# Performance work log

Measured on AMD Instinct MI355X. Metric: run time of the kernel, lower is better.

Reference implementation:

```python
import jax, jax.numpy as jnp
import numpy as np

HEAD = 16
NEG = -1.0e9


def setup_inputs() -> dict:
    key = jax.random.key(0)
    ks = jax.random.split(key, 8)
    B, S, D = 2, 2048, 1024
    scale = 1.0 / np.sqrt(D)
    inp = {
        "query": jax.random.normal(ks[0], (B, S, D), jnp.float32),
        "key": jax.random.normal(ks[1], (B, S, D), jnp.float32),
        "value": jax.random.normal(ks[2], (B, S, D), jnp.float32),
        "mask": jnp.ones((B, S, S), jnp.int32),
        "w_q": jax.random.normal(ks[3], (D, D), jnp.float32) * scale,
        "b_q": jnp.zeros((D,), jnp.float32),
        "w_k": jax.random.normal(ks[4], (D, D), jnp.float32) * scale,
        "b_k": jnp.zeros((D,), jnp.float32),
        "w_v": jax.random.normal(ks[5], (D, D), jnp.float32) * scale,
        "b_v": jnp.zeros((D,), jnp.float32),
        "w_o": jax.random.normal(ks[6], (D, D), jnp.float32) * scale,
        "b_o": jnp.zeros((D,), jnp.float32),
    }
    return inp


def _split_heads(x, B, S, H, dk):
    # [B,S,D] -> [B,H,S,dk]
    return x.reshape(B, S, H, dk).transpose(0, 2, 1, 3)


def reference(query, key, value, mask, w_q, b_q, w_k, b_k, w_v, b_v, w_o, b_o):
    B, S, D = query.shape
    H = HEAD
    dk = D // H
    q = _split_heads(query @ w_q.T + b_q, B, S, H, dk)
    k = _split_heads(key @ w_k.T + b_k, B, S, H, dk)
    v = _split_heads(value @ w_v.T + b_v, B, S, H, dk)
    # scores: [B,H,S,S]
    scores = jnp.einsum('bhqd,bhkd->bhqk', q, k) / jnp.sqrt(jnp.float32(dk))
    scores = jnp.where(mask[:, None, :, :] == 0, NEG, scores)
    p = jax.nn.softmax(scores, axis=-1)  # dropout is identity in eval
    x = jnp.einsum('bhqk,bhkd->bhqd', p, v)  # [B,H,S,dk]
    x = x.transpose(0, 2, 1, 3).reshape(B, S, D)
    return x @ w_o.T + b_o
```

## Files before the change

kernel.cpp:

```cpp
#include <hip/hip_runtime.h>
#include <hip/hip_bf16.h>

typedef float f32x4 __attribute__((ext_vector_type(4)));
typedef short bf16x8 __attribute__((ext_vector_type(8)));
typedef unsigned short u16x4 __attribute__((ext_vector_type(4)));

#define BB 2
#define SS 2048
#define DM 1024
#define NH 16
#define DKH 64
#define MROWS 4096

__device__ __forceinline__ unsigned short f2bf(float x) {
  union { float f; unsigned int u; } v; v.f = x;
  unsigned int r = v.u + 0x7fffu + ((v.u >> 16) & 1u);
  return (unsigned short)(r >> 16);
}

__device__ __forceinline__ void gll16(const void* g, void* l) {
  __builtin_amdgcn_global_load_lds(
      (const __attribute__((address_space(1))) void*)g,
      (__attribute__((address_space(3))) void*)l, 16, 0, 0);
}

template <int C>
__device__ __forceinline__ float dppf(float x) {
  return __builtin_bit_cast(float,
      __builtin_amdgcn_mov_dpp(__builtin_bit_cast(int, x), C, 0xf, 0xf, true));
}
__device__ __forceinline__ float rowsum16(float v) {
  v += dppf<0xB1>(v);
  v += dppf<0x4E>(v);
  v += dppf<0x141>(v);
  v += dppf<0x140>(v);
  return v;
}

struct CvtArgs {
  const float* src[7];
  unsigned short* dst[7];
  int n4[7];
  const int* mask;
  int* flags;
};

__global__ __launch_bounds__(256) void cvt_mask_kernel(CvtArgs a) {
  const int z = blockIdx.y;
  if (z == 7) {
    const int bid = blockIdx.x;
    if (bid >= 512) return;
    const int b = bid >> 8, qt = (bid >> 4) & 15, kt = bid & 15;
    __shared__ int sf;
    if (threadIdx.x == 0) sf = 0;
    __syncthreads();
    int any0 = 0;
    const size_t base = ((size_t)b * SS + qt * 128) * SS + kt * 128;
    for (int p = 0; p < 64; ++p) {
      int i = p * 256 + threadIdx.x;
      int r = i >> 7, col = i & 127;
      any0 |= (a.mask[base + (size_t)r * SS + col] == 0);
    }
    if (any0) sf = 1;
    __syncthreads();
    if (threadIdx.x == 0) a.flags[bid] = sf;
    return;
  }
  const int i = blockIdx.x * 256 + threadIdx.x;
  if (i >= a.n4[z]) return;
  f32x4 v = ((const f32x4*)a.src[z])[i];
  u16x4 o;
  o[0] = f2bf(v[0]); o[1] = f2bf(v[1]); o[2] = f2bf(v[2]); o[3] = f2bf(v[3]);
  ((u16x4*)a.dst[z])[i] = o;
}

struct ProjArgs {
  const unsigned short* A[3];
  const unsigned short* W[3];
  const float* bias[3];
  void* out[3];
  float alpha[3];
  int mode[3];
};

template <int TAG>
__global__ __launch_bounds__(256, 3) void proj_gemm(ProjArgs args) {
  __shared__ __align__(16) char pbuf[17408];
  unsigned short (*As)[32] = (unsigned short (*)[32])pbuf;
  unsigned short (*Bs)[32] = (unsigned short (*)[32])(pbuf + 8192);
  unsigned short (*T)[136] = (unsigned short (*)[136])pbuf;

  const int z = blockIdx.z;
  const unsigned short* __restrict__ A = args.A[z];
  const unsigned short* __restrict__ W = args.W[z];
  const float* __restrict__ bias = args.bias[z];
  const float alpha = args.alpha[z];
  const int mode = args.mode[z];

  const int tid = threadIdx.x;
  const int w = tid >> 6, lane = tid & 63;
  const int quad = lane >> 4, c = lane & 15;
  const int m0 = blockIdx.x * 128, n0 = blockIdx.y * 128;
  const int wm = (w >> 1) * 64, wn = (w & 1) * 64;
  const int sr = lane >> 2, scc = lane & 3;
  const int lx = scc ^ ((sr >> 1) & 3);
  const int sk = (quad ^ ((c >> 1) & 3)) * 8;

  f32x4 acc[4][4];
#pragma unroll
  for (int i = 0; i < 4; ++i)
#pragma unroll
    for (int j = 0; j < 4; ++j) { f32x4 zz = {0.f, 0.f, 0.f, 0.f}; acc[i][j] = zz; }

  for (int kt = 0; kt < 32; ++kt) {
    const int k0 = kt * 32;
    __syncthreads();
#pragma unroll
    for (int t = 0; t < 2; ++t) {
      const int tt = w + t * 4;
      const int r = tt * 16 + sr;
      gll16(A + (size_t)(m0 + r) * DM + k0 + lx * 8, &As[r][scc * 8]);
      gll16(W + (size_t)(n0 + r) * DM + k0 + lx * 8, &Bs[r][scc * 8]);
    }
    __syncthreads();
    bf16x8 af[4], bfr[4];
#pragma unroll
    for (int i = 0; i < 4; ++i) af[i] = *(const bf16x8*)&As[wm + i * 16 + c][sk];
#pragma unroll
    for (int j = 0; j < 4; ++j) bfr[j] = *(const bf16x8*)&Bs[wn + j * 16 + c][sk];
#pragma unroll
    for (int i = 0; i < 4; ++i)
#pragma unroll
      for (int j = 0; j < 4; ++j)
        acc[i][j] = __builtin_amdgcn_mfma_f32_16x16x32_bf16(af[i], bfr[j], acc[i][j], 0, 0, 0);
  }

  if (mode == 1) {
    unsigned short* outp = (unsigned short*)args.out[z];
    const int bb = m0 >> 11, sblk = (m0 >> 7) & 15;
#pragma unroll
    for (int h = 0; h < 2; ++h) {
      __syncthreads();
      if ((w & 1) == h) {
#pragma unroll
        for (int j = 0; j < 4; ++j) {
          const int row = j * 16 + c;
          const float bn = bias[n0 + h * 64 + row];
#pragma unroll
          for (int r = 0; r < 4; ++r) {
            u16x4 pkt;
#pragma unroll
            for (int i = 0; i < 4; ++i) pkt[i] = f2bf((acc[i][j][r] + bn) * alpha);
            *(u16x4*)&T[row][quad * 32 + r * 8 + (w >> 1) * 4] = pkt;
          }
        }
      }
      __syncthreads();
      const int row = tid >> 2, seg = tid & 3;
      const int n = n0 + h * 64 + row;
      const int hh = n >> 6, d = n & 63;
      const size_t gb = (((size_t)(bb * NH + hh)) * DKH + d) * SS + sblk * 128;
#pragma unroll
      for (int q = 0; q < 4; ++q)
        *(bf16x8*)&outp[gb + (seg + 4 * q) * 8] = *(const bf16x8*)&T[row][(seg + 4 * q) * 8];
    }
    return;
  }

#pragma unroll
  for (int i = 0; i < 4; ++i)
#pragma unroll
    for (int j = 0; j < 4; ++j)
#pragma unroll
      for (int r = 0; r < 4; ++r) {
        const int m = m0 + wm + i * 16 + quad * 4 + r;
        const int n = n0 + wn + j * 16 + c;
        const float val = (acc[i][j][r] + bias[n]) * alpha;
        if (mode == 2) {
          ((float*)args.out[z])[(size_t)m * DM + n] = val;
        } else {
          const int bb = m >> 11, s = m & 2047, hh = n >> 6, d = n & 63;
          const size_t idx = (((size_t)(bb * NH + hh)) * SS + s) * DKH + d;
          ((unsigned short*)args.out[z])[idx] = f2bf(val);
        }
      }
}

__global__ __launch_bounds__(256, 2) void attn_kernel(
    const unsigned short* __restrict__ qp, const unsigned short* __restrict__ kp,
    const unsigned short* __restrict__ vtp, const int* __restrict__ mask,
    const int* __restrict__ flags, unsigned short* __restrict__ xb) {
  __shared__ __align__(16) char smem[65536];
  unsigned short (*Ks)[128][32] = (unsigned short (*)[128][32])smem;
  unsigned short (*Vt)[64][32]  = (unsigned short (*)[64][32])(smem + 16384);
  unsigned short (*Qs)[128][32] = (unsigned short (*)[128][32])(smem + 32768);
  unsigned short (*Ps)[128]     = (unsigned short (*)[128])(smem + 32768);

  const int tid = threadIdx.x;
  const int w = tid >> 6, lane = tid & 63;
  const int quad = lane >> 4, c = lane & 15;
  const int qt = blockIdx.x, bh = blockIdx.y;
  const int b = bh >> 4, h = bh & 15;
  const int q0 = qt * 128;
  const int sr = lane >> 2, scc = lane & 3;
  const int lx = scc ^ ((sr >> 1) & 3);
  const int sk = (quad ^ ((c >> 1) & 3)) * 8;

#pragma unroll
  for (int t = 0; t < 4; ++t) {
    const int tt = w * 4 + t;
    const int kk = tt >> 3;
    const int r = (tt & 7) * 16 + sr;
    gll16(qp + ((size_t)bh * SS + q0 + r) * DKH + kk * 32 + lx * 8, &Qs[kk][r][scc * 8]);
  }
  __syncthreads();
  bf16x8 aq[2][2];
#pragma unroll
  for (int rt = 0; rt < 2; ++rt)
#pragma unroll
    for (int kk = 0; kk < 2; ++kk)
      aq[rt][kk] = *(const bf16x8*)&Qs[kk][w * 32 + rt * 16 + c][sk];

  f32x4 acco[2][4];
#pragma unroll
  for (int rt = 0; rt < 2; ++rt)
#pragma unroll
    for (int j = 0; j < 4; ++j) { f32x4 zz = {0.f, 0.f, 0.f, 0.f}; acco[rt][j] = zz; }
  float l_run[2][4];
#pragma unroll
  for (int rt = 0; rt < 2; ++rt)
#pragma unroll
    for (int r = 0; r < 4; ++r) l_run[rt][r] = 0.f;

  for (int kt = 0; kt < 16; ++kt) {
    const int k0 = kt * 128;
    __syncthreads();
#pragma unroll
    for (int i = 0; i < 4; ++i) {
      const int tt = w * 4 + i;
      {
        const int kk = tt >> 3, r = (tt & 7) * 16 + sr;
        gll16(kp + ((size_t)bh * SS + k0 + r) * DKH + kk * 32 + lx * 8, &Ks[kk][r][scc * 8]);
      }
      {
        const int kc = tt >> 2, d = (tt & 3) * 16 + sr;
        gll16(vtp + ((size_t)bh * DKH + d) * SS + k0 + kc * 32 + lx * 8, &Vt[kc][d][scc * 8]);
      }
    }
    __syncthreads();

    f32x4 accs[2][8];
#pragma unroll
    for (int rt = 0; rt < 2; ++rt)
#pragma unroll
      for (int j = 0; j < 8; ++j) { f32x4 zz = {0.f, 0.f, 0.f, 0.f}; accs[rt][j] = zz; }
#pragma unroll
    for (int j = 0; j < 8; ++j) {
      const int rowk = j * 16 + c;
      const bf16x8 bk0 = *(const bf16x8*)&Ks[0][rowk][sk];
      const bf16x8 bk1 = *(const bf16x8*)&Ks[1][rowk][sk];
#pragma unroll
      for (int rt = 0; rt < 2; ++rt) {
        accs[rt][j] = __builtin_amdgcn_mfma_f32_16x16x32_bf16(aq[rt][0], bk0, accs[rt][j], 0, 0, 0);
        accs[rt][j] = __builtin_amdgcn_mfma_f32_16x16x32_bf16(aq[rt][1], bk1, accs[rt][j], 0, 0, 0);
      }
    }

    if (flags[((size_t)b * 16 + qt) * 16 + kt]) {
#pragma unroll
      for (int rt = 0; rt < 2; ++rt)
#pragma unroll
        for (int j = 0; j < 8; ++j)
#pragma unroll
          for (int r = 0; r < 4; ++r) {
            const int qq = q0 + w * 32 + rt * 16 + quad * 4 + r;
            const int kk2 = k0 + j * 16 + c;
            if (mask[((size_t)b * SS + qq) * SS + kk2] == 0) accs[rt][j][r] = -1.0e30f;
          }
    }

#pragma unroll
    for (int rt = 0; rt < 2; ++rt)
#pragma unroll
      for (int r = 0; r < 4; ++r) {
        union { bf16x8 v8; __hip_bfloat162 h2[4]; } pk;
        float s = 0.f;
#pragma unroll
        for (int jj = 0; jj < 4; ++jj) {
          const float p0 = __builtin_amdgcn_exp2f(accs[rt][2 * jj][r]);
          const float p1 = __builtin_amdgcn_exp2f(accs[rt][2 * jj + 1][r]);
          float2 pp; pp.x = p0; pp.y = p1;
          pk.h2[jj] = __float22bfloat162_rn(pp);
          s += p0 + p1;
        }
        l_run[rt][r] += s;
        const int prow = w * 32 + rt * 16 + quad * 4 + r;
        *(bf16x8*)&Ps[prow][(c ^ ((prow >> 1) & 7)) * 8] = pk.v8;
      }

#pragma unroll
    for (int kc = 0; kc < 4; ++kc) {
      const int pc = ((kc * 4 + quad) ^ ((c >> 1) & 7)) * 8;
      const bf16x8 ap0 = *(const bf16x8*)&Ps[w * 32 + c][pc];
      const bf16x8 ap1 = *(const bf16x8*)&Ps[w * 32 + 16 + c][pc];
#pragma unroll
      for (int j = 0; j < 4; ++j) {
        const bf16x8 bv = *(const bf16x8*)&Vt[kc][j * 16 + c][sk];
        acco[0][j] = __builtin_amdgcn_mfma_f32_16x16x32_bf16(ap0, bv, acco[0][j], 0, 0, 0);
        acco[1][j] = __builtin_amdgcn_mfma_f32_16x16x32_bf16(ap1, bv, acco[1][j], 0, 0, 0);
      }
    }
  }

#pragma unroll
  for (int rt = 0; rt < 2; ++rt)
#pragma unroll
    for (int r = 0; r < 4; ++r) {
      const float inv = 1.0f / rowsum16(l_run[rt][r]);
      const int q = q0 + w * 32 + rt * 16 + quad * 4 + r;
#pragma unroll
      for (int j = 0; j < 4; ++j) {
        xb[((size_t)b * SS + q) * DM + h * DKH + j * 16 + c] = f2bf(acco[rt][j][r] * inv);
      }
    }
}

extern "C" void kernel_launch(void* const* d_in, const int* in_sizes, int n_in,
                              void* d_out, int out_size, void* d_ws, size_t ws_size,
                              hipStream_t stream) {
  (void)in_sizes; (void)n_in; (void)out_size; (void)ws_size;
  const float* query = (const float*)d_in[0];
  const float* key_  = (const float*)d_in[1];
  const float* value = (const float*)d_in[2];
  const int*   mask  = (const int*)d_in[3];
  const float* w_q = (const float*)d_in[4];
  const float* b_q = (const float*)d_in[5];
  const float* w_k = (const float*)d_in[6];
  const float* b_k = (const float*)d_in[7];
  const float* w_v = (const float*)d_in[8];
  const float* b_v = (const float*)d_in[9];
  const float* w_o = (const float*)d_in[10];
  const float* b_o = (const float*)d_in[11];

  char* ws = (char*)d_ws;
  const size_t SZ_IN = (size_t)MROWS * DM * 2;
  const size_t SZ_W  = (size_t)DM * DM * 2;
  unsigned short* qin = (unsigned short*)(ws);
  unsigned short* kin = (unsigned short*)(ws + SZ_IN);
  unsigned short* vin = (unsigned short*)(ws + 2 * SZ_IN);
  unsigned short* wqb = (unsigned short*)(ws + 3 * SZ_IN);
  unsigned short* wkb = (unsigned short*)(ws + 3 * SZ_IN + SZ_W);
  unsigned short* wvb = (unsigned short*)(ws + 3 * SZ_IN + 2 * SZ_W);
  unsigned short* wob = (unsigned short*)(ws + 3 * SZ_IN + 3 * SZ_W);
  unsigned short* qp  = (unsigned short*)(ws + 3 * SZ_IN + 4 * SZ_W);
  unsigned short* kp  = (unsigned short*)(ws + 4 * SZ_IN + 4 * SZ_W);
  unsigned short* vtp = (unsigned short*)(ws + 5 * SZ_IN + 4 * SZ_W);
  unsigned short* xb  = (unsigned short*)(ws + 6 * SZ_IN + 4 * SZ_W);
  int* flags          = (int*)(ws + 7 * SZ_IN + 4 * SZ_W);

  CvtArgs ca;
  ca.src[0] = query; ca.src[1] = key_; ca.src[2] = value;
  ca.src[3] = w_q; ca.src[4] = w_k; ca.src[5] = w_v; ca.src[6] = w_o;
  ca.dst[0] = qin; ca.dst[1] = kin; ca.dst[2] = vin;
  ca.dst[3] = wqb; ca.dst[4] = wkb; ca.dst[5] = wvb; ca.dst[6] = wob;
  ca.n4[0] = ca.n4[1] = ca.n4[2] = MROWS * DM / 4;
  ca.n4[3] = ca.n4[4] = ca.n4[5] = ca.n4[6] = DM * DM / 4;
  ca.mask = mask; ca.flags = flags;
  cvt_mask_kernel<<<dim3(4096, 8), 256, 0, stream>>>(ca);

  ProjArgs pa;
  pa.A[0] = qin; pa.A[1] = kin; pa.A[2] = vin;
  pa.W[0] = wqb; pa.W[1] = wkb; pa.W[2] = wvb;
  pa.bias[0] = b_q; pa.bias[1] = b_k; pa.bias[2] = b_v;
  pa.out[0] = qp; pa.out[1] = kp; pa.out[2] = vtp;
  pa.alpha[0] = 0.18033688011112042f; pa.alpha[1] = 1.f; pa.alpha[2] = 1.f;
  pa.mode[0] = 0; pa.mode[1] = 0; pa.mode[2] = 1;
  proj_gemm<0><<<dim3(32, 8, 3), 256, 0, stream>>>(pa);

  attn_kernel<<<dim3(16, 32), 256, 0, stream>>>(qp, kp, vtp, mask, flags, xb);

  ProjArgs po;
  po.A[0] = po.A[1] = po.A[2] = xb;
  po.W[0] = po.W[1] = po.W[2] = wob;
  po.bias[0] = po.bias[1] = po.bias[2] = b_o;
  po.out[0] = po.out[1] = po.out[2] = d_out;
  po.alpha[0] = po.alpha[1] = po.alpha[2] = 1.f;
  po.mode[0] = po.mode[1] = po.mode[2] = 2;
  proj_gemm<1><<<dim3(32, 8, 1), 256, 0, stream>>>(po);
}
```

Measured before the change: 263.3 us.

## Use BK=64 GEMM tiles, smaller M tile for output projection, flatten convert grid

The projection GEMM now stages K in chunks of 64 instead of 32, halving the number of barrier pairs per tile, with a new XOR swizzle for the wider LDS rows. The output projection uses a 64-row M tile, giving 512 blocks instead of 256 so more CUs are busy. The convert/mask kernel moves to a flat 1D grid sized exactly to the work, which removes the idle blocks of the old 2D grid. The cost is larger LDS use per block, which may reduce occupancy.

```diff
diff --git a/kernel.cpp b/kernel.cpp
--- a/kernel.cpp
+++ b/kernel.cpp
@@ -40,17 +40,15 @@
 struct CvtArgs {
   const float* src[7];
   unsigned short* dst[7];
-  int n4[7];
   const int* mask;
   int* flags;
 };
 
 __global__ __launch_bounds__(256) void cvt_mask_kernel(CvtArgs a) {
-  const int z = blockIdx.y;
-  if (z == 7) {
-    const int bid = blockIdx.x;
-    if (bid >= 512) return;
-    const int b = bid >> 8, qt = (bid >> 4) & 15, kt = bid & 15;
+  const int bid = blockIdx.x;
+  if (bid >= 16384) {
+    const int mb = bid - 16384;
+    const int b = mb >> 8, qt = (mb >> 4) & 15, kt = mb & 15;
     __shared__ int sf;
     if (threadIdx.x == 0) sf = 0;
     __syncthreads();
@@ -63,11 +61,12 @@
     }
     if (any0) sf = 1;
     __syncthreads();
-    if (threadIdx.x == 0) a.flags[bid] = sf;
+    if (threadIdx.x == 0) a.flags[mb] = sf;
     return;
   }
-  const int i = blockIdx.x * 256 + threadIdx.x;
-  if (i >= a.n4[z]) return;
+  int z, i;
+  if (bid < 12288) { z = bid >> 12; i = (bid & 4095) * 256 + threadIdx.x; }
+  else { z = 3 + ((bid - 12288) >> 10); i = ((bid - 12288) & 1023) * 256 + threadIdx.x; }
   f32x4 v = ((const f32x4*)a.src[z])[i];
   u16x4 o;
   o[0] = f2bf(v[0]); o[1] = f2bf(v[1]); o[2] = f2bf(v[2]); o[3] = f2bf(v[3]);
@@ -83,11 +82,13 @@
   int mode[3];
 };
 
-template <int TAG>
+template <int TAG, int MT>
 __global__ __launch_bounds__(256, 3) void proj_gemm(ProjArgs args) {
-  __shared__ __align__(16) char pbuf[17408];
-  unsigned short (*As)[32] = (unsigned short (*)[32])pbuf;
-  unsigned short (*Bs)[32] = (unsigned short (*)[32])(pbuf + 8192);
+  constexpr int NI = MT / 32;
+  constexpr int PBUF = MT * 128 + 16384;
+  __shared__ __align__(16) char pbuf[PBUF];
+  unsigned short (*As)[64] = (unsigned short (*)[64])pbuf;
+  unsigned short (*Bs)[64] = (unsigned short (*)[64])(pbuf + MT * 128);
   unsigned short (*T)[136] = (unsigned short (*)[136])pbuf;
 
   const int z = blockIdx.z;
@@ -100,75 +101,84 @@
   const int tid = threadIdx.x;
   const int w = tid >> 6, lane = tid & 63;
   const int quad = lane >> 4, c = lane & 15;
-  const int m0 = blockIdx.x * 128, n0 = blockIdx.y * 128;
-  const int wm = (w >> 1) * 64, wn = (w & 1) * 64;
-  const int sr = lane >> 2, scc = lane & 3;
-  const int lx = scc ^ ((sr >> 1) & 3);
-  const int sk = (quad ^ ((c >> 1) & 3)) * 8;
-
-  f32x4 acc[4][4];
-#pragma unroll
-  for (int i = 0; i < 4; ++i)
+  const int m0 = blockIdx.x * MT, n0 = blockIdx.y * 128;
+  const int wm = (w >> 1) * (MT / 2), wn = (w & 1) * 64;
+  const int s8r = lane >> 3, s8c = lane & 7;
+  const int g8 = (s8c ^ s8r) * 8;
+  const int cx = c & 7;
+
+  f32x4 acc[NI][4];
+#pragma unroll
+  for (int i = 0; i < NI; ++i)
 #pragma unroll
     for (int j = 0; j < 4; ++j) { f32x4 zz = {0.f, 0.f, 0.f, 0.f}; acc[i][j] = zz; }
 
-  for (int kt = 0; kt < 32; ++kt) {
-    const int k0 = kt * 32;
-    __syncthreads();
-#pragma unroll
-    for (int t = 0; t < 2; ++t) {
-      const int tt = w + t * 4;
-      const int r = tt * 16 + sr;
-      gll16(A + (size_t)(m0 + r) * DM + k0 + lx * 8, &As[r][scc * 8]);
-      gll16(W + (size_t)(n0 + r) * DM + k0 + lx * 8, &Bs[r][scc * 8]);
-    }
-    __syncthreads();
-    bf16x8 af[4], bfr[4];
-#pragma unroll
-    for (int i = 0; i < 4; ++i) af[i] = *(const bf16x8*)&As[wm + i * 16 + c][sk];
-#pragma unroll
-    for (int j = 0; j < 4; ++j) bfr[j] = *(const bf16x8*)&Bs[wn + j * 16 + c][sk];
-#pragma unroll
-    for (int i = 0; i < 4; ++i)
-#pragma unroll
-      for (int j = 0; j < 4; ++j)
-        acc[i][j] = __builtin_amdgcn_mfma_f32_16x16x32_bf16(af[i], bfr[j], acc[i][j], 0, 0, 0);
-  }
-
-  if (mode == 1) {
-    unsigned short* outp = (unsigned short*)args.out[z];
-    const int bb = m0 >> 11, sblk = (m0 >> 7) & 15;
-#pragma unroll
-    for (int h = 0; h < 2; ++h) {
-      __syncthreads();
-      if ((w & 1) == h) {
-#pragma unroll
-        for (int j = 0; j < 4; ++j) {
-          const int row = j * 16 + c;
-          const float bn = bias[n0 + h * 64 + row];
-#pragma unroll
-          for (int r = 0; r < 4; ++r) {
-            u16x4 pkt;
-#pragma unroll
-            for (int i = 0; i < 4; ++i) pkt[i] = f2bf((acc[i][j][r] + bn) * alpha);
-            *(u16x4*)&T[row][quad * 32 + r * 8 + (w >> 1) * 4] = pkt;
+  for (int kt = 0; kt < 16; ++kt) {
+    const int k0 = kt * 64;
+    __syncthreads();
+#pragma unroll
+    for (int t = 0; t < MT / 32; ++t) {
+      const int r = (w * (MT / 32) + t) * 8 + s8r;
+      gll16(A + (size_t)(m0 + r) * DM + k0 + g8, &As[r][s8c * 8]);
+    }
+#pragma unroll
+    for (int t = 0; t < 4; ++t) {
+      const int r = (w * 4 + t) * 8 + s8r;
+      gll16(W + (size_t)(n0 + r) * DM + k0 + g8, &Bs[r][s8c * 8]);
+    }
+    __syncthreads();
+#pragma unroll
+    for (int kk = 0; kk < 2; ++kk) {
+      const int po = ((quad ^ cx) ^ (kk * 4)) * 8;
+      bf16x8 af[NI], bfr[4];
+#pragma unroll
+      for (int i = 0; i < NI; ++i) af[i] = *(const bf16x8*)&As[wm + i * 16 + c][po];
+#pragma unroll
+      for (int j = 0; j < 4; ++j) bfr[j] = *(const bf16x8*)&Bs[wn + j * 16 + c][po];
+#pragma unroll
+      for (int i = 0; i < NI; ++i)
+#pragma unroll
+        for (int j = 0; j < 4; ++j)
+          acc[i][j] = __builtin_amdgcn_mfma_f32_16x16x32_bf16(af[i], bfr[j], acc[i][j], 0, 0, 0);
+    }
+  }
+
+  if constexpr (MT == 128) {
+    if (mode == 1) {
+      unsigned short* outp = (unsigned short*)args.out[z];
+      const int bb = m0 >> 11, sblk = (m0 >> 7) & 15;
+#pragma unroll
+      for (int h = 0; h < 2; ++h) {
+        __syncthreads();
+        if ((w & 1) == h) {
+#pragma unroll
+          for (int j = 0; j < 4; ++j) {
+            const int row = j * 16 + c;
+            const float bn = bias[n0 + h * 64 + row];
+#pragma unroll
+            for (int r = 0; r < 4; ++r) {
+              u16x4 pkt;
+#pragma unroll
+              for (int i = 0; i < 4; ++i) pkt[i] = f2bf((acc[i][j][r] + bn) * alpha);
+              *(u16x4*)&T[row][quad * 32 + r * 8 + (w >> 1) * 4] = pkt;
+            }
           }
         }
-      }
-      __syncthreads();
-      const int row = tid >> 2, seg = tid & 3;
-      const int n = n0 + h * 64 + row;
-      const int hh = n >> 6, d = n & 63;
-      const size_t gb = (((size_t)(bb * NH + hh)) * DKH + d) * SS + sblk * 128;
-#pragma unroll
-      for (int q = 0; q < 4; ++q)
-        *(bf16x8*)&outp[gb + (seg + 4 * q) * 8] = *(const bf16x8*)&T[row][(seg + 4 * q) * 8];
-    }
-    return;
-  }
-
-#pragma unroll
-  for (int i = 0; i < 4; ++i)
+        __syncthreads();
+        const int row = tid >> 2, seg = tid & 3;
+        const int n = n0 + h * 64 + row;
+        const int hh = n >> 6, d = n & 63;
+        const size_t gb = (((size_t)(bb * NH + hh)) * DKH + d) * SS + sblk * 128;
+#pragma unroll
+        for (int q = 0; q < 4; ++q)
+          *(bf16x8*)&outp[gb + (seg + 4 * q) * 8] = *(const bf16x8*)&T[row][(seg + 4 * q) * 8];
+      }
+      return;
+    }
+  }
+
+#pragma unroll
+  for (int i = 0; i < NI; ++i)
 #pragma unroll
     for (int j = 0; j < 4; ++j)
 #pragma unroll
@@ -363,10 +373,8 @@
   ca.src[3] = w_q; ca.src[4] = w_k; ca.src[5] = w_v; ca.src[6] = w_o;
   ca.dst[0] = qin; ca.dst[1] = kin; ca.dst[2] = vin;
   ca.dst[3] = wqb; ca.dst[4] = wkb; ca.dst[5] = wvb; ca.dst[6] = wob;
-  ca.n4[0] = ca.n4[1] = ca.n4[2] = MROWS * DM / 4;
-  ca.n4[3] = ca.n4[4] = ca.n4[5] = ca.n4[6] = DM * DM / 4;
   ca.mask = mask; ca.flags = flags;
-  cvt_mask_kernel<<<dim3(4096, 8), 256, 0, stream>>>(ca);
+  cvt_mask_kernel<<<dim3(16896), 256, 0, stream>>>(ca);
 
   ProjArgs pa;
   pa.A[0] = qin; pa.A[1] = kin; pa.A[2] = vin;
@@ -375,7 +383,7 @@
   pa.out[0] = qp; pa.out[1] = kp; pa.out[2] = vtp;
   pa.alpha[0] = 0.18033688011112042f; pa.alpha[1] = 1.f; pa.alpha[2] = 1.f;
   pa.mode[0] = 0; pa.mode[1] = 0; pa.mode[2] = 1;
-  proj_gemm<0><<<dim3(32, 8, 3), 256, 0, stream>>>(pa);
+  proj_gemm<0, 128><<<dim3(32, 8, 3), 256, 0, stream>>>(pa);
 
   attn_kernel<<<dim3(16, 32), 256, 0, stream>>>(qp, kp, vtp, mask, flags, xb);
 
@@ -386,5 +394,5 @@
   po.out[0] = po.out[1] = po.out[2] = d_out;
   po.alpha[0] = po.alpha[1] = po.alpha[2] = 1.f;
   po.mode[0] = po.mode[1] = po.mode[2] = 2;
-  proj_gemm<1><<<dim3(32, 8, 1), 256, 0, stream>>>(po);
-}
+  proj_gemm<1, 64><<<dim3(64, 8, 1), 256, 0, stream>>>(po);
+}
```

Result: faster. 254.3 us (-3.4%).
